# Optimization experiments

Measured on AMD Instinct MI355X. Metric: run time of the kernel, lower is better.

## Reference

```python
import jax, jax.numpy as jnp
import numpy as np

N, E = 50000, 600000
DIN, DMID, DATTR, DOUT, DEMB, DH, K = 128, 128, 32, 128, 256, 768, 16


def setup_inputs() -> dict:
    key = jax.random.key(0)
    ks = jax.random.split(key, 12)
    s = lambda d: 1.0 / np.sqrt(d)
    return {
        "x": jax.random.normal(ks[0], (N, DIN), jnp.float32),
        "attributes": jax.random.normal(ks[1], (N, DATTR), jnp.float32),
        "edge_weight": jax.random.uniform(ks[2], (E,), jnp.float32),
        "hidden_state": jax.random.normal(ks[3], (1, DH), jnp.float32),
        "edge_index": jax.random.randint(ks[4], (2, E), 0, N, jnp.int64),
        "W1": jax.random.normal(ks[5], (DIN, DMID), jnp.float32) * s(DIN),
        "b1": jnp.zeros((DMID,), jnp.float32),
        "W2": jax.random.normal(ks[6], (DMID + DATTR, DOUT), jnp.float32) * s(DMID + DATTR),
        "b2": jnp.zeros((DOUT,), jnp.float32),
        "Wmap": jax.random.normal(ks[7], (DOUT + DATTR, DEMB), jnp.float32) * s(DOUT + DATTR),
        "bmap": jnp.zeros((DEMB,), jnp.float32),
        "Wattn": jax.random.normal(ks[8], (DH, DOUT + DATTR), jnp.float32) * s(DH),
    }


def gcn_conv(x, W, b, src, dst, w, n):
    """PyG GCNConv with normalize=True: A_hat = D^-1/2 (A+I) D^-1/2, out = A_hat X W + b."""
    loop = jnp.arange(n, dtype=src.dtype)
    src2 = jnp.concatenate([src, loop])
    dst2 = jnp.concatenate([dst, loop])
    w2 = jnp.concatenate([w, jnp.ones((n,), x.dtype)])
    deg = jax.ops.segment_sum(w2, dst2, num_segments=n)
    dinv = jnp.where(deg > 0, jax.lax.rsqrt(jnp.maximum(deg, 1e-12)), 0.0)
    norm = dinv[src2] * w2 * dinv[dst2]        # [E+N]
    h = x @ W                                   # [n, out] transform first (small dim)
    msg = h[src2] * norm[:, None]               # gather + scale, [E+N, out]
    return jax.ops.segment_sum(msg, dst2, num_segments=n) + b


def reference(x, attributes, edge_weight, hidden_state, edge_index,
              W1, b1, W2, b2, Wmap, bmap, Wattn):
    n = x.shape[0]
    src, dst = edge_index[0], edge_index[1]
    h = jax.nn.relu(gcn_conv(x, W1, b1, src, dst, edge_weight, n))
    # F.dropout with training=False is identity (module run in eval mode)
    h = jnp.concatenate([h, attributes], axis=1)           # [N, DMID+DATTR]
    h = gcn_conv(h, W2, b2, src, dst, edge_weight, n)      # [N, DOUT]
    h = jnp.concatenate([h, attributes], axis=1)           # [N, DOUT+DATTR]
    # DotAttnChoseImportentNode: project hidden state, dot with node feats, take top-K nodes
    q = hidden_state @ Wattn                                # [1, DOUT+DATTR]
    scores = h @ q[0]                                       # [N]
    _, idx = jax.lax.top_k(scores, K)
    chose_nodes = h[idx].reshape(1, -1)                     # [1, K*(DOUT+DATTR)]
    # final_mapping: mean-pool graph embed + linear
    emb = jnp.mean(h, axis=0, keepdims=True) @ Wmap + bmap  # [1, DEMB]
    return jnp.concatenate([emb, chose_nodes], axis=1)      # [1, DEMB + K*(DOUT+DATTR)]
```

## Files before the change

### kernel.cpp

```cpp
#include <hip/hip_runtime.h>

#define N_NODES 50000
#define N_EDGES 600000
#define D_IN 128
#define D_MID 128
#define D_ATTR 32
#define D_OUT 128
#define D_EMB 256
#define D_H 768
#define K_TOP 16
#define D_CAT (D_OUT + D_ATTR)
#define N_CHUNKBLKS 196
#define N_CAND (N_CHUNKBLKS * K_TOP)
#define CSLOTS 13
#define WSCALE 262144.0f
#define CS_BLOCKS 768

__global__ void k_init(unsigned long long* packed, float* q) {
    int i = blockIdx.x * blockDim.x + threadIdx.x;
    if (i < N_NODES) packed[i] = 0ULL;
    if (i < D_CAT)   q[i] = 0.0f;
}

__global__ void k_deg(const int* __restrict__ dst, const float* __restrict__ w,
                      unsigned long long* __restrict__ packed) {
    int e = blockIdx.x * blockDim.x + threadIdx.x;
    if (e < N_EDGES) {
        int d = dst[e];
        unsigned long long q = (1ULL << 40)
                             + (unsigned long long)__float2uint_rn(w[e] * WSCALE);
        atomicAdd(&packed[d], q);
    }
}

__global__ void k_dinv(const unsigned long long* __restrict__ packed,
                       float* __restrict__ dinv, int* __restrict__ counts) {
    int i = blockIdx.x * blockDim.x + threadIdx.x;
    if (i < N_NODES) {
        unsigned long long p = packed[i];
        counts[i] = (int)(p >> 40);
        float wsum = (float)(p & 0xFFFFFFFFFFULL) * (1.0f / WSCALE);
        dinv[i] = rsqrtf(1.0f + wsum);
    }
}

__global__ __launch_bounds__(256) void k_scan_blk(const int* __restrict__ counts,
                                                  int* __restrict__ incl,
                                                  int* __restrict__ bsum) {
    __shared__ int sm[256];
    int tid = threadIdx.x;
    int i = blockIdx.x * 256 + tid;
    int v = (i < N_NODES) ? counts[i] : 0;
    sm[tid] = v;
    __syncthreads();
    for (int off = 1; off < 256; off <<= 1) {
        int t = (tid >= off) ? sm[tid - off] : 0;
        __syncthreads();
        sm[tid] += t;
        __syncthreads();
    }
    if (i < N_NODES) incl[i] = sm[tid];
    if (tid == 255) bsum[blockIdx.x] = sm[255];
}

__global__ __launch_bounds__(256) void k_scan_top(const int* __restrict__ bsum,
                                                  int* __restrict__ boff) {
    __shared__ int sm[256];
    int tid = threadIdx.x;
    int v = (tid < N_CHUNKBLKS) ? bsum[tid] : 0;
    sm[tid] = v;
    __syncthreads();
    for (int off = 1; off < 256; off <<= 1) {
        int t = (tid >= off) ? sm[tid - off] : 0;
        __syncthreads();
        sm[tid] += t;
        __syncthreads();
    }
    if (tid < N_CHUNKBLKS) boff[tid] = sm[tid] - v;
}

__global__ __launch_bounds__(256) void k_scan_add(const int* __restrict__ incl,
                                                  const int* __restrict__ boff,
                                                  const int* __restrict__ counts,
                                                  int* __restrict__ row_ptr,
                                                  int* __restrict__ cursor) {
    int i = blockIdx.x * 256 + threadIdx.x;
    if (i < N_NODES) {
        int ip = incl[i] + boff[blockIdx.x];
        row_ptr[i + 1] = ip;
        cursor[i] = ip - counts[i];
        if (i == 0) row_ptr[0] = 0;
    }
}

__global__ void k_fill(const int* __restrict__ src, const int* __restrict__ dst,
                       const float* __restrict__ w, const float* __restrict__ dinv,
                       int* __restrict__ cursor, int2* __restrict__ recs) {
    int e = blockIdx.x * blockDim.x + threadIdx.x;
    if (e < N_EDGES) {
        int s = src[e], d = dst[e];
        int pos = atomicAdd(&cursor[d], 1);
        float nr = dinv[s] * w[e] * dinv[d];
        recs[pos] = make_int2(s, __float_as_int(nr));
    }
}

#define GBM 128
#define GBK 32
__global__ __launch_bounds__(256) void k_gemm(
    const float* __restrict__ in1, int d1,
    const float* __restrict__ in2, int d2,
    const float* __restrict__ W,
    float* __restrict__ out)
{
    __shared__ float xs[GBM][GBK + 1];
    __shared__ float ws[GBK][128];
    int tid = threadIdx.x;
    int cx = tid & 7;
    int ry = tid >> 3;
    int row0 = blockIdx.x * GBM;
    float acc[4][16];
#pragma unroll
    for (int i = 0; i < 4; ++i)
#pragma unroll
        for (int j = 0; j < 16; ++j) acc[i][j] = 0.0f;
    int KD = d1 + d2;
    for (int kt = 0; kt < KD; kt += GBK) {
        const float* srcp; int sd, scol;
        if (kt < d1) { srcp = in1; sd = d1; scol = kt; }
        else         { srcp = in2; sd = d2; scol = kt - d1; }
#pragma unroll
        for (int i = 0; i < 4; ++i) {
            int vid = tid + i * 256;
            int rr = vid >> 3;
            int kc = (vid & 7) * 4;
            int r = row0 + rr;
            float4 val = make_float4(0.f, 0.f, 0.f, 0.f);
            if (r < N_NODES)
                val = *(const float4*)(srcp + (size_t)r * sd + scol + kc);
            xs[rr][kc + 0] = val.x;
            xs[rr][kc + 1] = val.y;
            xs[rr][kc + 2] = val.z;
            xs[rr][kc + 3] = val.w;
        }
#pragma unroll
        for (int i = 0; i < 4; ++i) {
            int vid = tid + i * 256;
            int kk = vid >> 5;
            int c = (vid & 31) * 4;
            *(float4*)&ws[kk][c] = *(const float4*)(W + (size_t)(kt + kk) * 128 + c);
        }
        __syncthreads();
#pragma unroll
        for (int kk = 0; kk < GBK; ++kk) {
            float xv[4];
#pragma unroll
            for (int i = 0; i < 4; ++i) xv[i] = xs[ry * 4 + i][kk];
            float wv[16];
            *(float4*)&wv[0]  = *(float4*)&ws[kk][cx * 16 + 0];
            *(float4*)&wv[4]  = *(float4*)&ws[kk][cx * 16 + 4];
            *(float4*)&wv[8]  = *(float4*)&ws[kk][cx * 16 + 8];
            *(float4*)&wv[12] = *(float4*)&ws[kk][cx * 16 + 12];
#pragma unroll
            for (int i = 0; i < 4; ++i)
#pragma unroll
                for (int j = 0; j < 16; ++j)
                    acc[i][j] += xv[i] * wv[j];
        }
        __syncthreads();
    }
#pragma unroll
    for (int i = 0; i < 4; ++i) {
        int r = row0 + ry * 4 + i;
        if (r < N_NODES) {
            float4* o = (float4*)(out + (size_t)r * 128 + cx * 16);
            o[0] = *(float4*)&acc[i][0];
            o[1] = *(float4*)&acc[i][4];
            o[2] = *(float4*)&acc[i][8];
            o[3] = *(float4*)&acc[i][12];
        }
    }
}

__global__ __launch_bounds__(256) void k_agg(
    const float* __restrict__ t, const float* __restrict__ dinv,
    const int* __restrict__ row_ptr, const int2* __restrict__ recs,
    const float* __restrict__ bias,
    float* __restrict__ out, int relu_flag,
    const float* __restrict__ attr, const float* __restrict__ q,
    float* __restrict__ scores, int score_flag)
{
    int lane = threadIdx.x & 63;
    int node = blockIdx.x * 4 + (threadIdx.x >> 6);
    if (node >= N_NODES) return;
    const float2* t2 = (const float2*)t;
    float di = dinv[node];
    float sw = di * di;
    float2 v = t2[(size_t)node * 64 + lane];
    float accx = v.x * sw, accy = v.y * sw;
    int e0 = row_ptr[node], e1 = row_ptr[node + 1];
    int len = e1 - e0;
    for (int base = 0; base < len; base += 64) {
        int m = len - base; if (m > 64) m = 64;
        int2 myrec = make_int2(0, 0);
        if (lane < m) myrec = recs[e0 + base + lane];
        int j = 0;
        for (; j + 4 <= m; j += 4) {
            int s0 = __shfl(myrec.x, j + 0, 64);
            int s1 = __shfl(myrec.x, j + 1, 64);
            int s2 = __shfl(myrec.x, j + 2, 64);
            int s3 = __shfl(myrec.x, j + 3, 64);
            float w0 = __int_as_float(__shfl(myrec.y, j + 0, 64));
            float w1 = __int_as_float(__shfl(myrec.y, j + 1, 64));
            float w2 = __int_as_float(__shfl(myrec.y, j + 2, 64));
            float w3 = __int_as_float(__shfl(myrec.y, j + 3, 64));
            float2 u0 = t2[(size_t)s0 * 64 + lane];
            float2 u1 = t2[(size_t)s1 * 64 + lane];
            float2 u2 = t2[(size_t)s2 * 64 + lane];
            float2 u3 = t2[(size_t)s3 * 64 + lane];
            accx += w0 * u0.x + w1 * u1.x + w2 * u2.x + w3 * u3.x;
            accy += w0 * u0.y + w1 * u1.y + w2 * u2.y + w3 * u3.y;
        }
        for (; j < m; ++j) {
            int s = __shfl(myrec.x, j, 64);
            float wn = __int_as_float(__shfl(myrec.y, j, 64));
            float2 u = t2[(size_t)s * 64 + lane];
            accx += wn * u.x;
            accy += wn * u.y;
        }
    }
    const float2* b2 = (const float2*)bias;
    float2 bb = b2[lane];
    accx += bb.x; accy += bb.y;
    if (relu_flag) {
        accx = fmaxf(accx, 0.0f);
        accy = fmaxf(accy, 0.0f);
    }
    float2 res; res.x = accx; res.y = accy;
    ((float2*)out)[(size_t)node * 64 + lane] = res;
    if (score_flag) {
        const float2* q2 = (const float2*)q;
        float2 qq = q2[lane];
        float s = accx * qq.x + accy * qq.y;
        if (lane < 16) {
            const float2* at2 = (const float2*)attr;
            float2 a = at2[(size_t)node * 16 + lane];
            float2 qa = q2[64 + lane];
            s += a.x * qa.x + a.y * qa.y;
        }
        for (int off = 32; off; off >>= 1) s += __shfl_xor(s, off, 64);
        if (lane == 0) scores[node] = s;
    }
}

__global__ void k_q(const float* __restrict__ hs, const float* __restrict__ Wattn,
                    float* __restrict__ q) {
    int j = threadIdx.x;
    if (j >= D_CAT) return;
    int k0 = blockIdx.x * (D_H / 8);
    float acc = 0.0f;
    for (int k = k0; k < k0 + D_H / 8; k++) acc += hs[k] * Wattn[k * D_CAT + j];
    atomicAdd(&q[j], acc);
}

__global__ __launch_bounds__(256) void k_colsum_partial(const float* __restrict__ h2,
                                                        const float* __restrict__ attr,
                                                        float* __restrict__ partial) {
    __shared__ float4 sm[256];
    int tid = threadIdx.x;
    int per = (N_NODES + CS_BLOCKS - 1) / CS_BLOCKS;
    int r0 = blockIdx.x * per;
    int r1 = min(N_NODES, r0 + per);
    float* myrow = partial + (size_t)blockIdx.x * D_CAT;
    {
        const float4* h4 = (const float4*)h2;
        int c = tid & 31;
        float4 acc = make_float4(0.f, 0.f, 0.f, 0.f);
        for (int r = r0 + (tid >> 5); r < r1; r += 8) {
            float4 v = h4[(size_t)r * 32 + c];
            acc.x += v.x; acc.y += v.y; acc.z += v.z; acc.w += v.w;
        }
        sm[tid] = acc;
        __syncthreads();
        if (tid < 32) {
            float4 s = sm[tid];
#pragma unroll
            for (int g = 1; g < 8; ++g) {
                float4 v = sm[g * 32 + tid];
                s.x += v.x; s.y += v.y; s.z += v.z; s.w += v.w;
            }
            ((float4*)myrow)[tid] = s;
        }
        __syncthreads();
    }
    {
        const float4* a4 = (const float4*)attr;
        int c = tid & 7;
        float4 acc = make_float4(0.f, 0.f, 0.f, 0.f);
        for (int r = r0 + (tid >> 3); r < r1; r += 32) {
            float4 v = a4[(size_t)r * 8 + c];
            acc.x += v.x; acc.y += v.y; acc.z += v.z; acc.w += v.w;
        }
        sm[tid] = acc;
        __syncthreads();
        if (tid < 8) {
            float4 s = sm[tid];
#pragma unroll
            for (int g = 1; g < 32; ++g) {
                float4 v = sm[g * 8 + tid];
                s.x += v.x; s.y += v.y; s.z += v.z; s.w += v.w;
            }
            ((float4*)(myrow + D_OUT))[tid] = s;
        }
    }
}

__global__ __launch_bounds__(256) void k_colsum_reduce(const float* __restrict__ partial,
                                                       float* __restrict__ colsum) {
    __shared__ float4 sm[256];
    int tid = threadIdx.x;
    int cg = blockIdx.x;
    float4 acc = make_float4(0.f, 0.f, 0.f, 0.f);
#pragma unroll
    for (int k = 0; k < 3; ++k) {
        int b = tid + k * 256;
        float4 v = *(const float4*)(partial + (size_t)b * D_CAT + cg * 4);
        acc.x += v.x; acc.y += v.y; acc.z += v.z; acc.w += v.w;
    }
    sm[tid] = acc;
    __syncthreads();
    for (int off = 128; off; off >>= 1) {
        if (tid < off) {
            float4 v = sm[tid + off];
            sm[tid].x += v.x; sm[tid].y += v.y; sm[tid].z += v.z; sm[tid].w += v.w;
        }
        __syncthreads();
    }
    if (tid == 0) *(float4*)(colsum + cg * 4) = sm[0];
}

__global__ __launch_bounds__(256) void k_top1(const float* __restrict__ scores,
                                              float* __restrict__ cand_s,
                                              int* __restrict__ cand_i) {
    __shared__ float ss[256];
    __shared__ int si[256];
    __shared__ float rs[256];
    __shared__ int ri[256];
    int tid = threadIdx.x;
    int i = blockIdx.x * 256 + tid;
    ss[tid] = (i < N_NODES) ? scores[i] : -INFINITY;
    si[tid] = i;
    __syncthreads();
    for (int it = 0; it < K_TOP; ++it) {
        rs[tid] = ss[tid]; ri[tid] = si[tid];
        __syncthreads();
        for (int off = 128; off; off >>= 1) {
            if (tid < off) {
                float s2 = rs[tid + off]; int i2 = ri[tid + off];
                if (s2 > rs[tid] || (s2 == rs[tid] && i2 < ri[tid])) { rs[tid] = s2; ri[tid] = i2; }
            }
            __syncthreads();
        }
        if (tid == 0) {
            cand_s[blockIdx.x * K_TOP + it] = rs[0];
            cand_i[blockIdx.x * K_TOP + it] = ri[0];
        }
        __syncthreads();
        if (si[tid] == ri[0]) ss[tid] = -INFINITY;
        __syncthreads();
    }
}

__global__ __launch_bounds__(256) void k_top2(const float* __restrict__ cand_s,
                                              const int* __restrict__ cand_i,
                                              int* __restrict__ topidx) {
    float s[CSLOTS]; int ix[CSLOTS];
    int tid = threadIdx.x;
    int lane = tid & 63;
    int wave = tid >> 6;
#pragma unroll
    for (int j = 0; j < CSLOTS; ++j) {
        int c = tid + j * 256;
        s[j]  = (c < N_CAND) ? cand_s[c] : -INFINITY;
        ix[j] = (c < N_CAND) ? cand_i[c] : 0x7fffffff;
    }
    __shared__ float wsum_s[4];
    __shared__ int   wsum_i[4];
    __shared__ int   win_i;
    for (int it = 0; it < K_TOP; ++it) {
        float bs = -INFINITY; int bi = 0x7fffffff;
#pragma unroll
        for (int j = 0; j < CSLOTS; ++j) {
            if (s[j] > bs || (s[j] == bs && ix[j] < bi)) { bs = s[j]; bi = ix[j]; }
        }
#pragma unroll
        for (int off = 32; off; off >>= 1) {
            float s2 = __shfl_xor(bs, off, 64);
            int   i2 = __shfl_xor(bi, off, 64);
            if (s2 > bs || (s2 == bs && i2 < bi)) { bs = s2; bi = i2; }
        }
        if (lane == 0) { wsum_s[wave] = bs; wsum_i[wave] = bi; }
        __syncthreads();
        if (tid == 0) {
            float ws0 = wsum_s[0]; int wi0 = wsum_i[0];
#pragma unroll
            for (int w = 1; w < 4; ++w) {
                float s2 = wsum_s[w]; int i2 = wsum_i[w];
                if (s2 > ws0 || (s2 == ws0 && i2 < wi0)) { ws0 = s2; wi0 = i2; }
            }
            win_i = wi0;
            topidx[it] = wi0;
        }
        __syncthreads();
        int w = win_i;
#pragma unroll
        for (int j = 0; j < CSLOTS; ++j)
            if (ix[j] == w) s[j] = -INFINITY;
        __syncthreads();
    }
}

__global__ __launch_bounds__(256) void k_emb_gather(
    const float* __restrict__ colsum, const float* __restrict__ Wmap,
    const float* __restrict__ bmap, const int* __restrict__ topidx,
    const float* __restrict__ h2, const float* __restrict__ attr,
    float* __restrict__ out)
{
    int tid = threadIdx.x;
    __shared__ float cs[D_CAT];
    if (tid < D_CAT) cs[tid] = colsum[tid];
    __syncthreads();
    float acc = 0.0f;
#pragma unroll 8
    for (int k = 0; k < D_CAT; ++k) acc += cs[k] * Wmap[k * D_EMB + tid];
    out[tid] = acc * (1.0f / N_NODES) + bmap[tid];
    __shared__ int ti[K_TOP];
    if (tid < K_TOP) ti[tid] = topidx[tid];
    __syncthreads();
    for (int idx = tid; idx < K_TOP * D_CAT; idx += 256) {
        int kk = idx / D_CAT;
        int d = idx % D_CAT;
        int node = ti[kk];
        out[D_EMB + idx] = (d < D_OUT) ? h2[node * D_OUT + d]
                                       : attr[node * D_ATTR + (d - D_OUT)];
    }
}

extern "C" void kernel_launch(void* const* d_in, const int* in_sizes, int n_in,
                              void* d_out, int out_size, void* d_ws, size_t ws_size,
                              hipStream_t stream) {
    const float* x      = (const float*)d_in[0];
    const float* attr   = (const float*)d_in[1];
    const float* ew     = (const float*)d_in[2];
    const float* hs     = (const float*)d_in[3];
    const int*   ei     = (const int*)d_in[4];
    const float* W1     = (const float*)d_in[5];
    const float* b1     = (const float*)d_in[6];
    const float* W2     = (const float*)d_in[7];
    const float* b2     = (const float*)d_in[8];
    const float* Wmap   = (const float*)d_in[9];
    const float* bmap   = (const float*)d_in[10];
    const float* Wattn  = (const float*)d_in[11];
    float* out = (float*)d_out;
    const int* e_src = ei;
    const int* e_dst = ei + N_EDGES;

    size_t off = 0;
    auto alloc = [&](size_t bytes) {
        void* p = (char*)d_ws + off;
        off += (bytes + 255) / 256 * 256;
        return p;
    };
    unsigned long long* packed = (unsigned long long*)alloc((size_t)N_NODES * 8);
    float* dinv   = (float*)alloc((size_t)N_NODES * 4);
    int*   counts = (int*)  alloc((size_t)N_NODES * 4);
    int*   rowp   = (int*)  alloc((size_t)(N_NODES + 1) * 4);
    int*   cursor = (int*)  alloc((size_t)N_NODES * 4);
    int2*  recs   = (int2*) alloc((size_t)N_EDGES * 8);
    float* bufA   = (float*)alloc((size_t)N_NODES * 128 * 4);
    float* bufB   = (float*)alloc((size_t)N_NODES * 128 * 4);
    float* scores = (float*)alloc((size_t)N_NODES * 4);
    float* q      = (float*)alloc(D_CAT * 4);
    float* colsum = (float*)alloc(D_CAT * 4);
    float* partial= (float*)alloc((size_t)CS_BLOCKS * D_CAT * 4);
    float* cand_s = (float*)alloc((size_t)N_CAND * 4);
    int*   cand_i = (int*)  alloc((size_t)N_CAND * 4);
    int*   incl   = (int*)  alloc((size_t)N_NODES * 4);
    int*   bsum   = (int*)  alloc((size_t)N_CHUNKBLKS * 4);
    int*   boff   = (int*)  alloc((size_t)N_CHUNKBLKS * 4);
    int*   topidx = (int*)  alloc((size_t)K_TOP * 4);

    int nblk = (N_NODES + 255) / 256;
    int eblk = (N_EDGES + 255) / 256;

    hipLaunchKernelGGL(k_init, dim3(nblk), dim3(256), 0, stream, packed, q);
    hipLaunchKernelGGL(k_deg, dim3(eblk), dim3(256), 0, stream, e_dst, ew, packed);
    hipLaunchKernelGGL(k_dinv, dim3(nblk), dim3(256), 0, stream, packed, dinv, counts);
    hipLaunchKernelGGL(k_scan_blk, dim3(nblk), dim3(256), 0, stream, counts, incl, bsum);
    hipLaunchKernelGGL(k_scan_top, dim3(1), dim3(256), 0, stream, bsum, boff);
    hipLaunchKernelGGL(k_scan_add, dim3(nblk), dim3(256), 0, stream, incl, boff, counts,
                       rowp, cursor);
    hipLaunchKernelGGL(k_fill, dim3(eblk), dim3(256), 0, stream, e_src, e_dst, ew, dinv,
                       cursor, recs);
    hipLaunchKernelGGL(k_q, dim3(8), dim3(192), 0, stream, hs, Wattn, q);
    hipLaunchKernelGGL(k_gemm, dim3((N_NODES + GBM - 1) / GBM), dim3(256), 0, stream,
                       x, D_IN, x, 0, W1, bufA);
    hipLaunchKernelGGL(k_agg, dim3((N_NODES + 3) / 4), dim3(256), 0, stream,
                       bufA, dinv, rowp, recs, b1, bufB, 1,
                       (const float*)nullptr, (const float*)nullptr, (float*)nullptr, 0);
    hipLaunchKernelGGL(k_gemm, dim3((N_NODES + GBM - 1) / GBM), dim3(256), 0, stream,
                       bufB, D_MID, attr, D_ATTR, W2, bufA);
    hipLaunchKernelGGL(k_agg, dim3((N_NODES + 3) / 4), dim3(256), 0, stream,
                       bufA, dinv, rowp, recs, b2, bufB, 0,
                       attr, q, scores, 1);
    hipLaunchKernelGGL(k_colsum_partial, dim3(CS_BLOCKS), dim3(256), 0, stream,
                       bufB, attr, partial);
    hipLaunchKernelGGL(k_colsum_reduce, dim3(D_CAT / 4), dim3(256), 0, stream,
                       partial, colsum);
    hipLaunchKernelGGL(k_top1, dim3(N_CHUNKBLKS), dim3(256), 0, stream,
                       scores, cand_s, cand_i);
    hipLaunchKernelGGL(k_top2, dim3(1), dim3(256), 0, stream, cand_s, cand_i, topidx);
    hipLaunchKernelGGL(k_emb_gather, dim3(1), dim3(256), 0, stream,
                       colsum, Wmap, bmap, topidx, bufB, attr, out);
}
```

Baseline: 324.6 us.

## Replace tiled GEMM with persistent shuffle-broadcast GEMM and unroll aggregation by eight

The shared-memory tiled GEMM is replaced with a persistent, templated kernel. Each block keeps the whole weight matrix in LDS, and each wave processes four rows at a time, broadcasting input values with wave shuffles. This drops the per-tile x staging and its barriers, but the inner loop needs four shuffles per two FMA pairs and reuses far less data per thread. Separately, the edge aggregation loop gains an 8-way unrolled path so more gathers are in flight at once.

```diff
diff --git a/kernel.cpp b/kernel.cpp
--- a/kernel.cpp
+++ b/kernel.cpp
@@ -105,80 +105,62 @@
     }
 }
 
-#define GBM 128
-#define GBK 32
-__global__ __launch_bounds__(256) void k_gemm(
-    const float* __restrict__ in1, int d1,
-    const float* __restrict__ in2, int d2,
+template<int KD>
+__global__ __launch_bounds__(256) void k_gemm_p(
+    const float* __restrict__ in1,
+    const float* __restrict__ in2,
     const float* __restrict__ W,
     float* __restrict__ out)
 {
-    __shared__ float xs[GBM][GBK + 1];
-    __shared__ float ws[GBK][128];
-    int tid = threadIdx.x;
-    int cx = tid & 7;
-    int ry = tid >> 3;
-    int row0 = blockIdx.x * GBM;
-    float acc[4][16];
-#pragma unroll
-    for (int i = 0; i < 4; ++i)
-#pragma unroll
-        for (int j = 0; j < 16; ++j) acc[i][j] = 0.0f;
-    int KD = d1 + d2;
-    for (int kt = 0; kt < KD; kt += GBK) {
-        const float* srcp; int sd, scol;
-        if (kt < d1) { srcp = in1; sd = d1; scol = kt; }
-        else         { srcp = in2; sd = d2; scol = kt - d1; }
-#pragma unroll
-        for (int i = 0; i < 4; ++i) {
-            int vid = tid + i * 256;
-            int rr = vid >> 3;
-            int kc = (vid & 7) * 4;
-            int r = row0 + rr;
-            float4 val = make_float4(0.f, 0.f, 0.f, 0.f);
-            if (r < N_NODES)
-                val = *(const float4*)(srcp + (size_t)r * sd + scol + kc);
-            xs[rr][kc + 0] = val.x;
-            xs[rr][kc + 1] = val.y;
-            xs[rr][kc + 2] = val.z;
-            xs[rr][kc + 3] = val.w;
-        }
-#pragma unroll
-        for (int i = 0; i < 4; ++i) {
-            int vid = tid + i * 256;
-            int kk = vid >> 5;
-            int c = (vid & 31) * 4;
-            *(float4*)&ws[kk][c] = *(const float4*)(W + (size_t)(kt + kk) * 128 + c);
-        }
-        __syncthreads();
-#pragma unroll
-        for (int kk = 0; kk < GBK; ++kk) {
-            float xv[4];
-#pragma unroll
-            for (int i = 0; i < 4; ++i) xv[i] = xs[ry * 4 + i][kk];
-            float wv[16];
-            *(float4*)&wv[0]  = *(float4*)&ws[kk][cx * 16 + 0];
-            *(float4*)&wv[4]  = *(float4*)&ws[kk][cx * 16 + 4];
-            *(float4*)&wv[8]  = *(float4*)&ws[kk][cx * 16 + 8];
-            *(float4*)&wv[12] = *(float4*)&ws[kk][cx * 16 + 12];
-#pragma unroll
-            for (int i = 0; i < 4; ++i)
-#pragma unroll
-                for (int j = 0; j < 16; ++j)
-                    acc[i][j] += xv[i] * wv[j];
-        }
-        __syncthreads();
-    }
-#pragma unroll
-    for (int i = 0; i < 4; ++i) {
-        int r = row0 + ry * 4 + i;
-        if (r < N_NODES) {
-            float4* o = (float4*)(out + (size_t)r * 128 + cx * 16);
-            o[0] = *(float4*)&acc[i][0];
-            o[1] = *(float4*)&acc[i][4];
-            o[2] = *(float4*)&acc[i][8];
-            o[3] = *(float4*)&acc[i][12];
-        }
+    __shared__ float ws[KD * 128];
+    int tid = threadIdx.x;
+    for (int i = tid; i < KD * 32; i += 256)
+        ((float4*)ws)[i] = ((const float4*)W)[i];
+    __syncthreads();
+    int lane = tid & 63;
+    int gw = blockIdx.x * 4 + (tid >> 6);
+    int nw = gridDim.x * 4;
+    constexpr int NSEG = (KD + 63) / 64;
+    for (int r0 = gw * 4; r0 < N_NODES; r0 += nw * 4) {
+        float xr[4][NSEG];
+#pragma unroll
+        for (int r = 0; r < 4; ++r) {
+            int rr = r0 + r;
+#pragma unroll
+            for (int s = 0; s < NSEG; ++s) {
+                float v = 0.0f;
+                if (s < 2) v = in1[(size_t)rr * 128 + s * 64 + lane];
+                else if (lane < 32) v = in2[(size_t)rr * 32 + lane];
+                xr[r][s] = v;
+            }
+        }
+        float a00 = 0.f, a01 = 0.f, a10 = 0.f, a11 = 0.f;
+        float a20 = 0.f, a21 = 0.f, a30 = 0.f, a31 = 0.f;
+#pragma unroll
+        for (int s = 0; s < NSEG; ++s) {
+            const int kmax = (s * 64 + 64 <= KD) ? 64 : (KD - s * 64);
+#pragma unroll
+            for (int ku = 0; ku < kmax; ++ku) {
+                int k = s * 64 + ku;
+                float x0 = __shfl(xr[0][s], ku, 64);
+                float x1 = __shfl(xr[1][s], ku, 64);
+                float x2 = __shfl(xr[2][s], ku, 64);
+                float x3 = __shfl(xr[3][s], ku, 64);
+                float2 wv = *(const float2*)&ws[k * 128 + lane * 2];
+                a00 += x0 * wv.x; a01 += x0 * wv.y;
+                a10 += x1 * wv.x; a11 += x1 * wv.y;
+                a20 += x2 * wv.x; a21 += x2 * wv.y;
+                a30 += x3 * wv.x; a31 += x3 * wv.y;
+            }
+        }
+        float2* o0 = (float2*)(out + (size_t)(r0 + 0) * 128 + lane * 2);
+        float2* o1 = (float2*)(out + (size_t)(r0 + 1) * 128 + lane * 2);
+        float2* o2 = (float2*)(out + (size_t)(r0 + 2) * 128 + lane * 2);
+        float2* o3 = (float2*)(out + (size_t)(r0 + 3) * 128 + lane * 2);
+        *o0 = make_float2(a00, a01);
+        *o1 = make_float2(a10, a11);
+        *o2 = make_float2(a20, a21);
+        *o3 = make_float2(a30, a31);
     }
 }
 
@@ -205,6 +187,32 @@
         int2 myrec = make_int2(0, 0);
         if (lane < m) myrec = recs[e0 + base + lane];
         int j = 0;
+        for (; j + 8 <= m; j += 8) {
+            int   s0 = __shfl(myrec.x, j + 0, 64), s1 = __shfl(myrec.x, j + 1, 64);
+            int   s2 = __shfl(myrec.x, j + 2, 64), s3 = __shfl(myrec.x, j + 3, 64);
+            int   s4 = __shfl(myrec.x, j + 4, 64), s5 = __shfl(myrec.x, j + 5, 64);
+            int   s6 = __shfl(myrec.x, j + 6, 64), s7 = __shfl(myrec.x, j + 7, 64);
+            float w0 = __int_as_float(__shfl(myrec.y, j + 0, 64));
+            float w1 = __int_as_float(__shfl(myrec.y, j + 1, 64));
+            float w2 = __int_as_float(__shfl(myrec.y, j + 2, 64));
+            float w3 = __int_as_float(__shfl(myrec.y, j + 3, 64));
+            float w4 = __int_as_float(__shfl(myrec.y, j + 4, 64));
+            float w5 = __int_as_float(__shfl(myrec.y, j + 5, 64));
+            float w6 = __int_as_float(__shfl(myrec.y, j + 6, 64));
+            float w7 = __int_as_float(__shfl(myrec.y, j + 7, 64));
+            float2 u0 = t2[(size_t)s0 * 64 + lane];
+            float2 u1 = t2[(size_t)s1 * 64 + lane];
+            float2 u2 = t2[(size_t)s2 * 64 + lane];
+            float2 u3 = t2[(size_t)s3 * 64 + lane];
+            float2 u4 = t2[(size_t)s4 * 64 + lane];
+            float2 u5 = t2[(size_t)s5 * 64 + lane];
+            float2 u6 = t2[(size_t)s6 * 64 + lane];
+            float2 u7 = t2[(size_t)s7 * 64 + lane];
+            accx += w0 * u0.x + w1 * u1.x + w2 * u2.x + w3 * u3.x
+                  + w4 * u4.x + w5 * u5.x + w6 * u6.x + w7 * u7.x;
+            accy += w0 * u0.y + w1 * u1.y + w2 * u2.y + w3 * u3.y
+                  + w4 * u4.y + w5 * u5.y + w6 * u6.y + w7 * u7.y;
+        }
         for (; j + 4 <= m; j += 4) {
             int s0 = __shfl(myrec.x, j + 0, 64);
             int s1 = __shfl(myrec.x, j + 1, 64);
@@ -503,13 +511,13 @@
     hipLaunchKernelGGL(k_fill, dim3(eblk), dim3(256), 0, stream, e_src, e_dst, ew, dinv,
                        cursor, recs);
     hipLaunchKernelGGL(k_q, dim3(8), dim3(192), 0, stream, hs, Wattn, q);
-    hipLaunchKernelGGL(k_gemm, dim3((N_NODES + GBM - 1) / GBM), dim3(256), 0, stream,
-                       x, D_IN, x, 0, W1, bufA);
+    hipLaunchKernelGGL((k_gemm_p<128>), dim3(512), dim3(256), 0, stream,
+                       x, x, W1, bufA);
     hipLaunchKernelGGL(k_agg, dim3((N_NODES + 3) / 4), dim3(256), 0, stream,
                        bufA, dinv, rowp, recs, b1, bufB, 1,
                        (const float*)nullptr, (const float*)nullptr, (float*)nullptr, 0);
-    hipLaunchKernelGGL(k_gemm, dim3((N_NODES + GBM - 1) / GBM), dim3(256), 0, stream,
-                       bufB, D_MID, attr, D_ATTR, W2, bufA);
+    hipLaunchKernelGGL((k_gemm_p<160>), dim3(512), dim3(256), 0, stream,
+                       bufB, attr, W2, bufA);
     hipLaunchKernelGGL(k_agg, dim3((N_NODES + 3) / 4), dim3(256), 0, stream,
                        bufA, dinv, rowp, recs, b2, bufB, 0,
                        attr, q, scores, 1);
```

New measurement: 721.3 us. 122% more time.
